# Optimization experiments

Measured on AMD Instinct MI355X. Metric: run time of the kernel, lower is better.

Reference implementation:

```python
import jax, jax.numpy as jnp
from jax import lax
import numpy as np

B, C_IN, C_OUT, H, W = 4, 256, 256, 64, 64
P = 4
DM = C_IN // P            # 64, d_model per parallel chunk
D_STATE = 16
D_CONV = 4
EXPAND = 2
D_INNER = EXPAND * DM     # 128
DT_RANK = max(1, -(-DM // 16))  # ceil(64/16) = 4


def setup_inputs() -> dict:
    key = jax.random.key(0)
    ks = jax.random.split(key, 12)
    s = lambda k, shape, scale=0.02: (jax.random.normal(k, shape, jnp.float32) * scale)
    dt = jax.random.uniform(ks[5], (D_INNER,), jnp.float32, 1e-3, 0.1)
    dt_bias = jnp.log(jnp.expm1(dt))  # inverse softplus, as in mamba_ssm init
    A_log = jnp.log(jnp.tile(jnp.arange(1, D_STATE + 1, dtype=jnp.float32), (D_INNER, 1)))
    return {
        "x": jax.random.normal(ks[0], (B, C_IN, H, W), jnp.float32),
        "ln_g": jnp.ones((C_IN,), jnp.float32),
        "ln_b": jnp.zeros((C_IN,), jnp.float32),
        "in_proj_w": s(ks[1], (2 * D_INNER, DM)),
        "conv_w": s(ks[2], (D_INNER, D_CONV), 0.1),
        "conv_b": jnp.zeros((D_INNER,), jnp.float32),
        "x_proj_w": s(ks[3], (DT_RANK + 2 * D_STATE, D_INNER)),
        "dt_proj_w": s(ks[4], (D_INNER, DT_RANK), 0.1),
        "dt_proj_b": dt_bias,
        "A_log": A_log,
        "D": jnp.ones((D_INNER,), jnp.float32),
        "out_proj_w": s(ks[6], (DM, D_INNER)),
        "skip_scale": jnp.ones((1,), jnp.float32),
        "proj_w": s(ks[7], (C_OUT, C_IN)),
        "proj_b": jnp.zeros((C_OUT,), jnp.float32),
        "cdc_w": s(ks[8], (C_OUT, 1, 3, 3), 0.1),      # depthwise 3x3, groups=C_OUT
        "theta_w": jnp.zeros((1, C_OUT), jnp.float32),  # nn.init.constant_(weight, 0)
        "theta_b": jnp.full((1,), -2.0, jnp.float32),   # nn.init.constant_(bias, -2)
        "pw_w": s(ks[9], (C_OUT, C_OUT)),               # 1x1 pointwise conv, no bias
    }


def _layernorm(x, g, b, eps=1e-5):
    mu = x.mean(-1, keepdims=True)
    var = ((x - mu) ** 2).mean(-1, keepdims=True)
    return (x - mu) * lax.rsqrt(var + eps) * g + b


def _mamba(x, in_proj_w, conv_w, conv_b, x_proj_w, dt_proj_w, dt_proj_b, A_log, D, out_proj_w):
    # x: [Bm, L, DM]
    xz = jnp.einsum('bld,ed->ble', x, in_proj_w)          # [Bm, L, 2*D_INNER]
    xc, z = jnp.split(xz, 2, axis=-1)
    # causal depthwise conv1d along L
    xt = jnp.swapaxes(xc, 1, 2)                           # [Bm, D_INNER, L]
    xt = lax.conv_general_dilated(xt, conv_w[:, None, :], (1,), [(D_CONV - 1, 0)],
                                  dimension_numbers=('NCH', 'OIH', 'NCH'),
                                  feature_group_count=D_INNER)
    xt = xt + conv_b[None, :, None]
    xs = jax.nn.silu(jnp.swapaxes(xt, 1, 2))              # [Bm, L, D_INNER]
    x_dbl = jnp.einsum('bld,ed->ble', xs, x_proj_w)       # [Bm, L, DT_RANK+2*D_STATE]
    dt, Bmat, Cmat = jnp.split(x_dbl, [DT_RANK, DT_RANK + D_STATE], axis=-1)
    delta = jax.nn.softplus(jnp.einsum('blr,dr->bld', dt, dt_proj_w) + dt_proj_b)
    A = -jnp.exp(A_log)                                   # [D_INNER, D_STATE]

    def step(h, inp):
        d_t, b_t, c_t, u_t = inp                          # [Bm,di],[Bm,ds],[Bm,ds],[Bm,di]
        h = h * jnp.exp(d_t[..., None] * A) + (d_t * u_t)[..., None] * b_t[:, None, :]
        return h, jnp.einsum('bds,bs->bd', h, c_t)

    h0 = jnp.zeros((x.shape[0], D_INNER, D_STATE), x.dtype)
    xs_t = (jnp.swapaxes(delta, 0, 1), jnp.swapaxes(Bmat, 0, 1),
            jnp.swapaxes(Cmat, 0, 1), jnp.swapaxes(xs, 0, 1))
    _, ys = lax.scan(step, h0, xs_t)                      # ys: [L, Bm, D_INNER]
    y = jnp.swapaxes(ys, 0, 1) + xs * D
    y = y * jax.nn.silu(z)
    return jnp.einsum('bld,od->blo', y, out_proj_w)       # [Bm, L, DM]


def reference(x, ln_g, ln_b, in_proj_w, conv_w, conv_b, x_proj_w, dt_proj_w, dt_proj_b,
              A_log, D, out_proj_w, skip_scale, proj_w, proj_b, cdc_w, theta_w, theta_b, pw_w):
    Bb, C = x.shape[:2]
    Hh, Ww = x.shape[2], x.shape[3]
    L = Hh * Ww
    x_flat = jnp.swapaxes(x.reshape(Bb, C, L), 1, 2)      # [B, L, C]
    x_norm = _layernorm(x_flat, ln_g, ln_b)
    # chunk along channel dim into P pieces, run shared Mamba on all as one big batch
    xc = jnp.moveaxis(x_norm.reshape(Bb, L, P, DM), 2, 0).reshape(P * Bb, L, DM)
    ym = _mamba(xc, in_proj_w, conv_w, conv_b, x_proj_w, dt_proj_w, dt_proj_b,
                A_log, D, out_proj_w) + skip_scale * xc
    ym = jnp.moveaxis(ym.reshape(P, Bb, L, DM), 0, 2).reshape(Bb, L, C)
    ym = _layernorm(ym, ln_g, ln_b)                       # same norm params (shared)
    yp = jnp.einsum('blc,oc->blo', ym, proj_w) + proj_b
    out = jnp.swapaxes(yp, 1, 2).reshape(Bb, C_OUT, Hh, Ww)
    # A_CDC: depthwise 3x3 conv + central-difference term
    out_normal = lax.conv_general_dilated(out, cdc_w, (1, 1), [(1, 1), (1, 1)],
                                          dimension_numbers=('NCHW', 'OIHW', 'NCHW'),
                                          feature_group_count=C_OUT)
    ksum = cdc_w.sum(axis=(2, 3))[:, 0]                   # [C_OUT]; depthwise 1x1 == scale
    edge = out_normal - out * ksum[None, :, None, None]
    theta = jax.nn.sigmoid(jnp.einsum('bchw,oc->bohw', out, theta_w)
                           + theta_b[None, :, None, None])
    cdc_out = out_normal + theta * edge
    g = jax.nn.gelu(cdc_out, approximate=False)           # nn.GELU exact
    cnn_out = jnp.einsum('bchw,oc->bohw', g, pw_w)        # 1x1 conv, no bias
    return out + cnn_out
```

## Files before the change

kernel.cpp:

```cpp
#include <hip/hip_runtime.h>
#include <hip/hip_bf16.h>
#include <math.h>

typedef __hip_bfloat16 bf16;
typedef short bf8_t __attribute__((ext_vector_type(8)));
typedef float f4_t  __attribute__((ext_vector_type(4)));
typedef float f2_t  __attribute__((ext_vector_type(2)));
#define MFMA16(a,b,c) __builtin_amdgcn_mfma_f32_16x16x32_bf16(a,b,c,0,0,0)
#define DEV __device__ __forceinline__

DEV float bf2f(bf16 h){ return __bfloat162float(h); }
DEV bf16 f2bf(float f){ return __float2bfloat16(f); }
DEV float ld(const void* p, size_t i, int md){
  return md ? ((const float*)p)[i] : bf2f(((const bf16*)p)[i]);
}
DEV float wred(float v){
  #pragma unroll
  for(int off=32; off>0; off>>=1) v += __shfl_down(v, off, 64);
  return __shfl(v, 0, 64);
}

__global__ __launch_bounds__(256) void k_detect(const unsigned short* __restrict__ xr, int* __restrict__ flag){
  __shared__ float sm[4];
  int t = threadIdx.x;
  float m = 0.f;
  for(int i=t;i<8192;i+=256){
    unsigned int w = ((unsigned int)xr[i]) << 16;
    float v = fabsf(__uint_as_float(w));
    if(v != v) v = 1e30f;
    m = fmaxf(m, v);
  }
  #pragma unroll
  for(int off=32; off>0; off>>=1) m = fmaxf(m, __shfl_down(m, off, 64));
  if((t & 63) == 0) sm[t >> 6] = m;
  __syncthreads();
  if(t == 0){
    float mm = fmaxf(fmaxf(sm[0], sm[1]), fmaxf(sm[2], sm[3]));
    *flag = (mm > 1e10f) ? 1 : 0;
  }
}

__global__ __launch_bounds__(256) void k_wcvt(const void* __restrict__ inw, const void* __restrict__ outw,
                                              const void* __restrict__ projw, const void* __restrict__ pww,
                                              bf16* __restrict__ dst, const int* __restrict__ modep){
  const int md = *modep;
  int g = blockIdx.x*256 + threadIdx.x;
  if(g >= 155648) return;
  const void* src; int i;
  if(g < 16384){ src = inw;   i = g; }
  else if(g < 24576){ src = outw;  i = g - 16384; }
  else if(g < 90112){ src = projw; i = g - 24576; }
  else { src = pww; i = g - 90112; }
  dst[g] = f2bf(ld(src, (size_t)i, md));
}

__global__ __launch_bounds__(256) void k_ln1(const void* __restrict__ x, const void* __restrict__ gam,
                                             const void* __restrict__ bet, bf16* __restrict__ xnb,
                                             const int* __restrict__ modep){
  __shared__ float sh[64*257];
  __shared__ float mus[64], rss[64];
  const int md = *modep;
  int t = threadIdx.x;
  int b = blockIdx.x >> 6, lt = blockIdx.x & 63;
  int l0 = lt << 6;
  int lane = t & 63, cg = t >> 6;
  size_t xbase = ((size_t)b << 20) + l0 + lane;
  if(md){
    const float* xp = (const float*)x + xbase;
    #pragma unroll 8
    for(int c = cg; c < 256; c += 4)
      sh[lane*257 + c] = xp[(size_t)c << 12];
  } else {
    const bf16* xp = (const bf16*)x + xbase;
    #pragma unroll 8
    for(int c = cg; c < 256; c += 4)
      sh[lane*257 + c] = bf2f(xp[(size_t)c << 12]);
  }
  __syncthreads();
  {
    int row = t >> 2, q = t & 3;
    const float* rp = sh + row*257 + q*64;
    float s = 0.f, s2 = 0.f;
    #pragma unroll 8
    for(int i=0;i<64;i++){ float v = rp[i]; s += v; s2 += v*v; }
    s  += __shfl_xor(s, 1, 64);  s2 += __shfl_xor(s2, 1, 64);
    s  += __shfl_xor(s, 2, 64);  s2 += __shfl_xor(s2, 2, 64);
    if(q == 0){
      float mu = s*(1.f/256.f);
      mus[row] = mu;
      rss[row] = rsqrtf(s2*(1.f/256.f) - mu*mu + 1e-5f);
    }
  }
  __syncthreads();
  int r0 = (t >> 6) << 4;
  #pragma unroll
  for(int k=0;k<4;k++){
    int c = (t & 63) + (k << 6);
    float gv = ld(gam, c, md), bv = ld(bet, c, md);
    #pragma unroll 4
    for(int rr=0; rr<16; rr++){
      int row = r0 + rr;
      xnb[((size_t)(b*4096 + l0 + row))*256 + c] =
        f2bf((sh[row*257 + c] - mus[row])*rss[row]*gv + bv);
    }
  }
}

__global__ __launch_bounds__(256) void k_inproj(const bf16* __restrict__ xnb, const bf16* __restrict__ wb,
                                                bf16* __restrict__ xcb, bf16* __restrict__ zb){
  __shared__ bf16 As[64*72];
  __shared__ bf16 Ws[256*72];
  int t = threadIdx.x;
  int bm = blockIdx.x >> 6, lt = blockIdx.x & 63;
  int p = bm >> 2, b = bm & 3, l0 = lt << 6;
  #pragma unroll
  for(int pass=0; pass<2; pass++){
    int idx = t + pass*256, r = idx >> 3, ch = idx & 7;
    *(uint4*)&As[r*72 + ch*8] = *(const uint4*)&xnb[((size_t)(b*4096 + l0 + r))*256 + p*64 + ch*8];
  }
  #pragma unroll
  for(int pass=0; pass<8; pass++){
    int idx = t + pass*256, e = idx >> 3, ch = idx & 7;
    *(uint4*)&Ws[e*72 + ch*8] = *(const uint4*)&wb[(size_t)e*64 + ch*8];
  }
  __syncthreads();
  int lane = t & 63, w = t >> 6, quad = lane >> 4, lr = lane & 15;
  f4_t acc[16];
  #pragma unroll
  for(int nt=0;nt<16;nt++) acc[nt] = (f4_t){0.f,0.f,0.f,0.f};
  #pragma unroll
  for(int kk=0; kk<64; kk+=32){
    bf8_t a = *(const bf8_t*)&As[(w*16 + lr)*72 + kk + quad*8];
    #pragma unroll
    for(int nt=0;nt<16;nt++){
      bf8_t bb = *(const bf8_t*)&Ws[(nt*16 + lr)*72 + kk + quad*8];
      acc[nt] = MFMA16(a, bb, acc[nt]);
    }
  }
  __syncthreads();
  bf16* Sl = Ws;
  #pragma unroll
  for(int nt=0;nt<16;nt++)
    #pragma unroll
    for(int r=0;r<4;r++)
      Sl[(w*16 + quad*4 + r)*264 + nt*16 + lr] = f2bf(acc[nt][r]);
  __syncthreads();
  #pragma unroll
  for(int pass=0; pass<8; pass++){
    int idx = t + pass*256, l = idx >> 5, c16 = idx & 31;
    int e0 = c16*8;
    uint4 v = *(uint4*)&Sl[l*264 + e0];
    size_t row = (size_t)bm*4096 + l0 + l;
    if(e0 < 128) *(uint4*)&xcb[row*128 + e0] = v;
    else         *(uint4*)&zb[row*128 + e0 - 128] = v;
  }
}

__global__ __launch_bounds__(256) void k_conv(const bf16* __restrict__ xcb, const void* __restrict__ cw,
                                              const void* __restrict__ cb, bf16* __restrict__ xsb,
                                              const int* __restrict__ modep){
  const int md = *modep;
  int g = blockIdx.x*256 + threadIdx.x;
  int d = g & 127;
  int t4 = g >> 7;
  int l4 = t4 & 1023;
  int bm = t4 >> 10;
  int l0 = l4 << 2;
  size_t base = ((size_t)bm*4096 + l0)*128 + d;
  const bf16* p = xcb + base;
  float w0 = ld(cw,(size_t)(d<<2)+0,md), w1 = ld(cw,(size_t)(d<<2)+1,md);
  float w2 = ld(cw,(size_t)(d<<2)+2,md), w3 = ld(cw,(size_t)(d<<2)+3,md);
  float bv = ld(cb,(size_t)d,md);
  float xm3, xm2, xm1;
  if(l4 > 0){ xm3 = bf2f(p[-384]); xm2 = bf2f(p[-256]); xm1 = bf2f(p[-128]); }
  else      { xm3 = 0.f; xm2 = 0.f; xm1 = 0.f; }
  float x0 = bf2f(p[0]), x1 = bf2f(p[128]), x2 = bf2f(p[256]), x3 = bf2f(p[384]);
  float y0 = fmaf(w0,xm3, fmaf(w1,xm2, fmaf(w2,xm1, fmaf(w3,x0, bv))));
  float y1 = fmaf(w0,xm2, fmaf(w1,xm1, fmaf(w2,x0,  fmaf(w3,x1, bv))));
  float y2 = fmaf(w0,xm1, fmaf(w1,x0,  fmaf(w2,x1,  fmaf(w3,x2, bv))));
  float y3 = fmaf(w0,x0,  fmaf(w1,x1,  fmaf(w2,x2,  fmaf(w3,x3, bv))));
  bf16* o = xsb + base;
  o[0]   = f2bf(y0 / (1.f + __expf(-y0)));
  o[128] = f2bf(y1 / (1.f + __expf(-y1)));
  o[256] = f2bf(y2 / (1.f + __expf(-y2)));
  o[384] = f2bf(y3 / (1.f + __expf(-y3)));
}

#define PTREE2(P, e1) \
  float e2s=(e1)*(e1), e4s=e2s*e2s, e8s=e4s*e4s; \
  f2_t P##0={(e1),e2s}; \
  f2_t P##1=P##0*(f2_t){e2s,e2s}; \
  f2_t e4v_={e4s,e4s}; f2_t P##2=P##0*e4v_, P##3=P##1*e4v_; \
  f2_t e8v_={e8s,e8s}; f2_t P##4=P##0*e8v_, P##5=P##1*e8v_, P##6=P##2*e8v_, P##7=P##3*e8v_;

__global__ __launch_bounds__(256) void k_cxs1(const bf16* __restrict__ xsb, const void* __restrict__ xpw,
                                              float* __restrict__ xdbl,
                                              const void* __restrict__ dtw, const void* __restrict__ dtb,
                                              const void* __restrict__ Alog,
                                              float* __restrict__ CP, bf16* __restrict__ CSb,
                                              const int* __restrict__ modep){
  __shared__ bf16 As[64*136];
  __shared__ bf16 Ws[64*136];
  float* sh = (float*)Ws;
  const int md = *modep;
  int t = threadIdx.x;
  int bm = blockIdx.x >> 6, lt = blockIdx.x & 63;
  size_t row0g = (size_t)bm*4096 + (lt << 6);
  #pragma unroll
  for(int pass=0; pass<4; pass++){
    int idx = t + pass*256, r = idx >> 4, ch = idx & 15;
    *(uint4*)&As[r*136 + ch*8] = *(const uint4*)&xsb[(row0g + r)*128 + ch*8];
  }
  for(int idx = t; idx < 8192; idx += 256){
    int e = idx >> 7, k = idx & 127;
    Ws[e*136 + k] = (e < 36) ? f2bf(ld(xpw, (size_t)e*128 + k, md)) : f2bf(0.f);
  }
  __syncthreads();
  int lane = t & 63, w = t >> 6, quad = lane >> 4, lr = lane & 15;
  f4_t acc[3];
  #pragma unroll
  for(int nt=0;nt<3;nt++) acc[nt] = (f4_t){0.f,0.f,0.f,0.f};
  #pragma unroll
  for(int kk=0; kk<128; kk+=32){
    bf8_t a = *(const bf8_t*)&As[(w*16 + lr)*136 + kk + quad*8];
    #pragma unroll
    for(int nt=0;nt<3;nt++){
      bf8_t bb = *(const bf8_t*)&Ws[(nt*16 + lr)*136 + kk + quad*8];
      acc[nt] = MFMA16(a, bb, acc[nt]);
    }
  }
  __syncthreads();
  #pragma unroll
  for(int nt=0;nt<3;nt++){
    int e = nt*16 + lr;
    if(e < 36){
      #pragma unroll
      for(int r=0;r<4;r++){
        int row = w*16 + quad*4 + r;
        float v = acc[nt][r];
        sh[row*36 + e] = v;
        xdbl[(row0g + row)*36 + e] = v;
      }
    }
  }
  int d = t & 127, chunk = t >> 7;
  float A[16];
  #pragma unroll
  for(int s=0;s<16;s++) A[s] = -expf(ld(Alog, (size_t)((d<<4)+s), md));
  float A0 = A[0];
  int fastf = 1;
  #pragma unroll
  for(int s=0;s<16;s++){
    float n = (float)(s+1);
    if(fabsf(A[s] - n*A0) > 2e-3f*fabsf(n*A0)) fastf = 0;
  }
  fastf = __all(fastf);
  float wdt[4];
  #pragma unroll
  for(int j=0;j<4;j++) wdt[j] = ld(dtw, (size_t)((d<<2)+j), md);
  float bdt = ld(dtb, (size_t)d, md);
  __syncthreads();
  f2_t h2[8];
  #pragma unroll
  for(int j=0;j<8;j++) h2[j] = (f2_t){0.f,0.f};
  float sumd = 0.f;
  const float* shc = sh + chunk*32*36;
  const bf16* uc = As + chunk*32*136;
  if(fastf){
    #pragma unroll
    for(int tt=0;tt<32;tt++){
      const float* r = shc + tt*36;
      float4 dt4 = *(const float4*)r;
      float v = fmaf(dt4.x,wdt[0], fmaf(dt4.y,wdt[1], fmaf(dt4.z,wdt[2], fmaf(dt4.w,wdt[3], bdt))));
      float dv = fmaxf(v,0.f) + __logf(1.f + __expf(-fabsf(v)));
      float u = bf2f(uc[tt*136 + d]);
      float du = dv*u; sumd += dv;
      const f2_t* B2 = (const f2_t*)(r+4);
      float e1 = __expf(dv*A0);
      PTREE2(p, e1);
      f2_t du2 = {du,du};
      h2[0] = h2[0]*p0 + du2*B2[0];
      h2[1] = h2[1]*p1 + du2*B2[1];
      h2[2] = h2[2]*p2 + du2*B2[2];
      h2[3] = h2[3]*p3 + du2*B2[3];
      h2[4] = h2[4]*p4 + du2*B2[4];
      h2[5] = h2[5]*p5 + du2*B2[5];
      h2[6] = h2[6]*p6 + du2*B2[6];
      h2[7] = h2[7]*p7 + du2*B2[7];
    }
  } else {
    for(int tt=0;tt<32;tt++){
      const float* r = shc + tt*36;
      float4 dt4 = *(const float4*)r;
      float v = fmaf(dt4.x,wdt[0], fmaf(dt4.y,wdt[1], fmaf(dt4.z,wdt[2], fmaf(dt4.w,wdt[3], bdt))));
      float dv = fmaxf(v,0.f) + __logf(1.f + __expf(-fabsf(v)));
      float u = bf2f(uc[tt*136 + d]);
      float du = dv*u; sumd += dv;
      const float* Bp = r + 4;
      #pragma unroll
      for(int j=0;j<8;j++){
        f2_t e = { __expf(dv*A[2*j]), __expf(dv*A[2*j+1]) };
        f2_t bb = { Bp[2*j], Bp[2*j+1] };
        h2[j] = h2[j]*e + (f2_t){du,du}*bb;
      }
    }
  }
  int c = lt*2 + chunk;
  size_t ob = ((size_t)(bm*128 + c)*128 + d) << 4;
  if(fastf){
    float qv = __expf(sumd*A0);
    PTREE2(P, qv);
    *(f2_t*)&CP[ob+ 0]=P0; *(f2_t*)&CP[ob+ 2]=P1; *(f2_t*)&CP[ob+ 4]=P2; *(f2_t*)&CP[ob+ 6]=P3;
    *(f2_t*)&CP[ob+ 8]=P4; *(f2_t*)&CP[ob+10]=P5; *(f2_t*)&CP[ob+12]=P6; *(f2_t*)&CP[ob+14]=P7;
  } else {
    #pragma unroll
    for(int s=0;s<16;s++) CP[ob+s] = __expf(sumd*A[s]);
  }
  __align__(16) bf16 pk[8];
  #pragma unroll
  for(int j=0;j<4;j++){ pk[2*j] = f2bf(h2[j].x); pk[2*j+1] = f2bf(h2[j].y); }
  *(uint4*)&CSb[ob] = *(uint4*)pk;
  #pragma unroll
  for(int j=0;j<4;j++){ pk[2*j] = f2bf(h2[4+j].x); pk[2*j+1] = f2bf(h2[4+j].y); }
  *(uint4*)&CSb[ob+8] = *(uint4*)pk;
}

__global__ __launch_bounds__(64) void k_scan2(float* __restrict__ CP, const bf16* __restrict__ CSb){
  int g = blockIdx.x*64 + threadIdx.x;
  int bm = g >> 11, ds = g & 2047;
  size_t base = ((size_t)bm << 18) + ds;
  float Pb[8], Sb[8];
  #pragma unroll
  for(int j=0;j<8;j++){
    size_t idx = base + ((size_t)j << 11);
    Pb[j] = CP[idx]; Sb[j] = bf2f(CSb[idx]);
  }
  float h = 0.f;
  #pragma unroll
  for(int grp=0; grp<16; grp++){
    float Pc[8], Sc[8];
    #pragma unroll
    for(int j=0;j<8;j++){ Pc[j]=Pb[j]; Sc[j]=Sb[j]; }
    if(grp < 15){
      #pragma unroll
      for(int j=0;j<8;j++){
        size_t idx = base + ((size_t)((grp+1)*8 + j) << 11);
        Pb[j] = CP[idx]; Sb[j] = bf2f(CSb[idx]);
      }
    }
    #pragma unroll
    for(int j=0;j<8;j++){
      size_t idx = base + ((size_t)(grp*8 + j) << 11);
      CP[idx] = h;
      h = fmaf(Pc[j], h, Sc[j]);
    }
  }
}

__global__ __launch_bounds__(128) void k_scan3(bf16* __restrict__ zb, const bf16* __restrict__ xsb,
                                               const float* __restrict__ xdbl,
                                               const void* __restrict__ dtw, const void* __restrict__ dtb,
                                               const void* __restrict__ Alog, const void* __restrict__ Dw,
                                               const float* __restrict__ CP, const int* __restrict__ modep){
  __shared__ float sh[32*36];
  __shared__ bf16 su[32*128];
  const int md = *modep;
  int d = threadIdx.x;
  int bm = blockIdx.x >> 7, c = blockIdx.x & 127;
  size_t row0 = (size_t)bm*4096 + (c<<5);
  {
    const float4* src = (const float4*)(xdbl + row0*36);
    for(int idx = d; idx < 288; idx += 128) ((float4*)sh)[idx] = src[idx];
    const uint4* gu = (const uint4*)(xsb + row0*128);
    uint4* lu = (uint4*)su;
    #pragma unroll
    for(int j=0;j<4;j++) lu[d + j*128] = gu[d + j*128];
  }
  float A[16];
  #pragma unroll
  for(int s=0;s<16;s++) A[s] = -expf(ld(Alog, (size_t)((d<<4)+s), md));
  float A0 = A[0];
  int fastf = 1;
  #pragma unroll
  for(int s=0;s<16;s++){
    float n = (float)(s+1);
    if(fabsf(A[s] - n*A0) > 2e-3f*fabsf(n*A0)) fastf = 0;
  }
  fastf = __all(fastf);
  float wdt[4];
  #pragma unroll
  for(int j=0;j<4;j++) wdt[j] = ld(dtw, (size_t)((d<<2)+j), md);
  float bdt = ld(dtb, (size_t)d, md);
  float Dd = ld(Dw, (size_t)d, md);
  size_t hb = ((size_t)(bm*128 + c)*128 + d) << 4;
  f2_t h2[8];
  #pragma unroll
  for(int j=0;j<8;j++) h2[j] = *(const f2_t*)&CP[hb + 2*j];
  __syncthreads();
  if(fastf){
    #pragma unroll
    for(int tt=0;tt<32;tt++){
      const float* r = sh + tt*36;
      size_t bg = (row0 + tt)*128 + d;
      float zv = bf2f(zb[bg]);
      float4 dt4 = *(const float4*)r;
      float v = fmaf(dt4.x,wdt[0], fmaf(dt4.y,wdt[1], fmaf(dt4.z,wdt[2], fmaf(dt4.w,wdt[3], bdt))));
      float dv = fmaxf(v,0.f) + __logf(1.f + __expf(-fabsf(v)));
      float u  = bf2f(su[tt*128 + d]);
      float du = dv*u;
      const f2_t* B2 = (const f2_t*)(r+4);
      const f2_t* C2 = (const f2_t*)(r+20);
      float e1 = __expf(dv*A0);
      PTREE2(p, e1);
      f2_t du2 = {du,du};
      f2_t ya = {0.f,0.f}, yb = {0.f,0.f};
      h2[0] = h2[0]*p0 + du2*B2[0];  ya += h2[0]*C2[0];
      h2[1] = h2[1]*p1 + du2*B2[1];  yb += h2[1]*C2[1];
      h2[2] = h2[2]*p2 + du2*B2[2];  ya += h2[2]*C2[2];
      h2[3] = h2[3]*p3 + du2*B2[3];  yb += h2[3]*C2[3];
      h2[4] = h2[4]*p4 + du2*B2[4];  ya += h2[4]*C2[4];
      h2[5] = h2[5]*p5 + du2*B2[5];  yb += h2[5]*C2[5];
      h2[6] = h2[6]*p6 + du2*B2[6];  ya += h2[6]*C2[6];
      h2[7] = h2[7]*p7 + du2*B2[7];  yb += h2[7]*C2[7];
      float y = (ya.x + ya.y) + (yb.x + yb.y);
      float yv = (y + u*Dd) * (zv / (1.f + __expf(-zv)));
      zb[bg] = f2bf(yv);
    }
  } else {
    for(int tt=0;tt<32;tt++){
      const float* r = sh + tt*36;
      size_t bg = (row0 + tt)*128 + d;
      float zv = bf2f(zb[bg]);
      float4 dt4 = *(const float4*)r;
      float v = fmaf(dt4.x,wdt[0], fmaf(dt4.y,wdt[1], fmaf(dt4.z,wdt[2], fmaf(dt4.w,wdt[3], bdt))));
      float dv = fmaxf(v,0.f) + __logf(1.f + __expf(-fabsf(v)));
      float u  = bf2f(su[tt*128 + d]);
      float du = dv*u;
      const float* Bp = r + 4;
      const float* Cp = r + 20;
      f2_t ya = {0.f,0.f};
      #pragma unroll
      for(int j=0;j<8;j++){
        f2_t e = { __expf(dv*A[2*j]), __expf(dv*A[2*j+1]) };
        f2_t bb = { Bp[2*j], Bp[2*j+1] };
        f2_t cc = { Cp[2*j], Cp[2*j+1] };
        h2[j] = h2[j]*e + (f2_t){du,du}*bb;
        ya += h2[j]*cc;
      }
      float y = ya.x + ya.y;
      float yv = (y + u*Dd) * (zv / (1.f + __expf(-zv)));
      zb[bg] = f2bf(yv);
    }
  }
}

__global__ __launch_bounds__(256) void k_outproj(const bf16* __restrict__ yb, const bf16* __restrict__ xnb,
                                                 const bf16* __restrict__ wb, const void* __restrict__ ss,
                                                 bf16* __restrict__ ymb, const int* __restrict__ modep){
  __shared__ bf16 As[64*72];
  __shared__ bf16 Ws[64*72];
  const int md = *modep;
  int t = threadIdx.x;
  int bm = blockIdx.x >> 6, lt = blockIdx.x & 63;
  int p = bm >> 2, b = bm & 3, l0 = lt << 6;
  int lane = t & 63, w = t >> 6, quad = lane >> 4, lr = lane & 15;
  f4_t acc[4];
  #pragma unroll
  for(int nt=0;nt<4;nt++) acc[nt] = (f4_t){0.f,0.f,0.f,0.f};
  for(int kb=0; kb<2; kb++){
    if(kb) __syncthreads();
    int k0 = kb << 6;
    #pragma unroll
    for(int pass=0; pass<2; pass++){
      int idx = t + pass*256, r = idx >> 3, ch = idx & 7;
      *(uint4*)&As[r*72 + ch*8] = *(const uint4*)&yb[((size_t)bm*4096 + l0 + r)*128 + k0 + ch*8];
    }
    #pragma unroll
    for(int pass=0; pass<2; pass++){
      int idx = t + pass*256, o = idx >> 3, ch = idx & 7;
      *(uint4*)&Ws[o*72 + ch*8] = *(const uint4*)&wb[(size_t)o*128 + k0 + ch*8];
    }
    __syncthreads();
    #pragma unroll
    for(int kk=0; kk<64; kk+=32){
      bf8_t a = *(const bf8_t*)&As[(w*16 + lr)*72 + kk + quad*8];
      #pragma unroll
      for(int nt=0;nt<4;nt++){
        bf8_t bb = *(const bf8_t*)&Ws[(nt*16 + lr)*72 + kk + quad*8];
        acc[nt] = MFMA16(a, bb, acc[nt]);
      }
    }
  }
  __syncthreads();
  bf16* Sl = As;
  #pragma unroll
  for(int nt=0;nt<4;nt++)
    #pragma unroll
    for(int r=0;r<4;r++)
      Sl[(w*16 + quad*4 + r)*72 + nt*16 + lr] = f2bf(acc[nt][r]);
  __syncthreads();
  float sv = ld(ss, 0, md);
  #pragma unroll
  for(int pass=0; pass<2; pass++){
    int idx = t + pass*256, l = idx >> 3, ch = idx & 7;
    size_t gi = ((size_t)b*4096 + l0 + l)*256 + p*64 + ch*8;
    uint4 yv = *(uint4*)&Sl[l*72 + ch*8];
    uint4 xv = *(const uint4*)&xnb[gi];
    const bf16* y8 = (const bf16*)&yv;
    const bf16* x8 = (const bf16*)&xv;
    uint4 ov; bf16* o8 = (bf16*)&ov;
    #pragma unroll
    for(int j=0;j<8;j++) o8[j] = f2bf(fmaf(sv, bf2f(x8[j]), bf2f(y8[j])));
    *(uint4*)&ymb[gi] = ov;
  }
}

__global__ __launch_bounds__(256) void k_ln2(bf16* __restrict__ ymb, const void* __restrict__ gam,
                                             const void* __restrict__ bet, const int* __restrict__ modep){
  const int md = *modep;
  int lane = threadIdx.x & 63, wv = threadIdx.x >> 6;
  size_t row = (size_t)blockIdx.x*4 + wv;
  bf16* rp = ymb + row*256 + (lane<<2);
  __align__(8) bf16 raw[4];
  *(ushort4*)raw = *(const ushort4*)rp;
  float v[4];
  #pragma unroll
  for(int i=0;i<4;i++) v[i] = bf2f(raw[i]);
  float s = v[0]+v[1]+v[2]+v[3];
  float s2 = v[0]*v[0]+v[1]*v[1]+v[2]*v[2]+v[3]*v[3];
  s = wred(s); s2 = wred(s2);
  float mu = s*(1.f/256.f);
  float rs = rsqrtf(s2*(1.f/256.f) - mu*mu + 1e-5f);
  int c = lane << 2;
  #pragma unroll
  for(int i=0;i<4;i++) raw[i] = f2bf((v[i]-mu)*rs*ld(gam,c+i,md) + ld(bet,c+i,md));
  *(ushort4*)rp = *(ushort4*)raw;
}

__global__ __launch_bounds__(256) void k_proj(const bf16* __restrict__ ymb, const bf16* __restrict__ wb,
                                              const void* __restrict__ pb, bf16* __restrict__ outbb,
                                              const void* __restrict__ tw, const void* __restrict__ tb2,
                                              float* __restrict__ theta, const int* __restrict__ modep){
  __shared__ bf16 As[32*72];
  __shared__ bf16 Ws[256*72];
  const int md = *modep;
  int t = threadIdx.x;
  int row0 = blockIdx.x << 5;
  int b = row0 >> 12, l0 = row0 & 4095;
  int lane = t & 63, w = t >> 6, quad = lane >> 4, lr = lane & 15;
  int rg = w & 1, ch2 = w >> 1;
  f4_t acc[8];
  #pragma unroll
  for(int nt=0;nt<8;nt++) acc[nt] = (f4_t){0.f,0.f,0.f,0.f};
  for(int kb=0; kb<4; kb++){
    if(kb) __syncthreads();
    int k0 = kb << 6;
    { int r = t >> 3, ch = t & 7;
      *(uint4*)&As[r*72 + ch*8] = *(const uint4*)&ymb[((size_t)(row0 + r))*256 + k0 + ch*8]; }
    #pragma unroll
    for(int pass=0; pass<8; pass++){
      int idx = t + pass*256, e = idx >> 3, ch = idx & 7;
      *(uint4*)&Ws[e*72 + ch*8] = *(const uint4*)&wb[(size_t)e*256 + k0 + ch*8];
    }
    __syncthreads();
    #pragma unroll
    for(int kk=0; kk<64; kk+=32){
      bf8_t a = *(const bf8_t*)&As[(rg*16 + lr)*72 + kk + quad*8];
      #pragma unroll
      for(int nt=0;nt<8;nt++){
        bf8_t bb = *(const bf8_t*)&Ws[(ch2*128 + nt*16 + lr)*72 + kk + quad*8];
        acc[nt] = MFMA16(a, bb, acc[nt]);
      }
    }
  }
  __syncthreads();
  bf16* Sl = Ws;
  #pragma unroll
  for(int nt=0;nt<8;nt++){
    int o = ch2*128 + nt*16 + lr;
    float bv = ld(pb, (size_t)o, md);
    #pragma unroll
    for(int r=0;r<4;r++)
      Sl[o*40 + rg*16 + quad*4 + r] = f2bf(acc[nt][r] + bv);
  }
  __syncthreads();
  #pragma unroll
  for(int pass=0; pass<4; pass++){
    int idx = t + pass*256, o = idx >> 2, q = idx & 3;
    uint4 v = *(uint4*)&Sl[o*40 + q*8];
    *(uint4*)&outbb[((size_t)(b*256 + o) << 12) + l0 + q*8] = v;
  }
  if(t < 32){
    float acc2 = 0.f;
    #pragma unroll 8
    for(int o=0;o<256;o++)
      acc2 = fmaf(bf2f(Sl[o*40 + t]), ld(tw, (size_t)o, md), acc2);
    float v = acc2 + ld(tb2, 0, md);
    theta[((size_t)b << 12) + l0 + t] = 1.f / (1.f + __expf(-v));
  }
}

__global__ __launch_bounds__(256) void k_cdc(const bf16* __restrict__ outbb, const float* __restrict__ theta,
                                             const void* __restrict__ cw, bf16* __restrict__ gbufb,
                                             const int* __restrict__ modep){
  const int md = *modep;
  int g = blockIdx.x*256 + threadIdx.x;
  int w4 = g & 15;
  int h0 = (g >> 4) & 63;
  int c  = (g >> 10) & 255;
  int b  = g >> 18;
  int w0 = w4 << 2;
  float wk[9]; float ks = 0.f;
  #pragma unroll
  for(int j=0;j<9;j++){ wk[j] = ld(cw, (size_t)c*9 + j, md); ks += wk[j]; }
  const bf16* base = outbb + (((size_t)b*256 + c) << 12);
  float X[3][6];
  #pragma unroll
  for(int dy=0;dy<3;dy++){
    int hh = h0 + dy - 1;
    #pragma unroll
    for(int dx=0;dx<6;dx++){
      int ww = w0 + dx - 1;
      X[dy][dx] = (hh>=0 && hh<64 && ww>=0 && ww<64) ? bf2f(base[(hh<<6)+ww]) : 0.f;
    }
  }
  float4 th = *(const float4*)&theta[((size_t)b<<12) + (h0<<6) + w0];
  float thv[4] = {th.x, th.y, th.z, th.w};
  __align__(8) bf16 outp[4];
  #pragma unroll
  for(int k=0;k<4;k++){
    float on = 0.f;
    #pragma unroll
    for(int dy=0;dy<3;dy++)
      #pragma unroll
      for(int dx=0;dx<3;dx++)
        on = fmaf(X[dy][k+dx], wk[dy*3+dx], on);
    float ctr  = X[1][k+1];
    float edge = on - ctr*ks;
    float cd   = fmaf(thv[k], edge, on);
    outp[k] = f2bf(0.5f * cd * (1.f + erff(cd * 0.70710678118654752f)));
  }
  *(ushort4*)&gbufb[(((size_t)b*256 + c) << 12) + (h0<<6) + w0] = *(ushort4*)outp;
}

__global__ __launch_bounds__(256) void k_pw(const bf16* __restrict__ gbufb, const bf16* __restrict__ outbb,
                                            const bf16* __restrict__ wb, void* __restrict__ outp,
                                            const int* __restrict__ modep){
  __shared__ bf16 As[64*72];
  __shared__ bf16 Bs[128*72];
  const int md = *modep;
  int t = threadIdx.x;
  int b  = blockIdx.x >> 7;
  int ot = (blockIdx.x >> 5) & 3;
  int ht = blockIdx.x & 31;
  int o0 = ot << 6, hw0 = ht << 7;
  int lane = t & 63, w = t >> 6, quad = lane >> 4, lr = lane & 15;
  f4_t acc[8];
  #pragma unroll
  for(int nt=0;nt<8;nt++) acc[nt] = (f4_t){0.f,0.f,0.f,0.f};
  for(int kb=0; kb<4; kb++){
    if(kb) __syncthreads();
    int k0 = kb << 6;
    #pragma unroll
    for(int pass=0; pass<2; pass++){
      int idx = t + pass*256, r = idx >> 3, ch = idx & 7;
      *(uint4*)&As[r*72 + ch*8] = *(const uint4*)&wb[(size_t)(o0 + r)*256 + k0 + ch*8];
    }
    #pragma unroll
    for(int pass=0; pass<4; pass++){
      int idx = t + pass*256, cc = idx >> 4, hc = idx & 15;
      uint4 gv = *(const uint4*)&gbufb[((size_t)(b*256 + k0 + cc) << 12) + hw0 + hc*8];
      const bf16* g8 = (const bf16*)&gv;
      #pragma unroll
      for(int j=0;j<8;j++) Bs[(hc*8 + j)*72 + cc] = g8[j];
    }
    __syncthreads();
    #pragma unroll
    for(int kk=0; kk<64; kk+=32){
      bf8_t a = *(const bf8_t*)&As[(w*16 + lr)*72 + kk + quad*8];
      #pragma unroll
      for(int nt=0;nt<8;nt++){
        bf8_t bb = *(const bf8_t*)&Bs[(nt*16 + lr)*72 + kk + quad*8];
        acc[nt] = MFMA16(a, bb, acc[nt]);
      }
    }
  }
  __syncthreads();
  bf16* Sl = Bs;
  #pragma unroll
  for(int nt=0;nt<8;nt++)
    #pragma unroll
    for(int r=0;r<4;r++)
      Sl[(w*16 + quad*4 + r)*136 + nt*16 + lr] = f2bf(acc[nt][r]);
  __syncthreads();
  #pragma unroll
  for(int pass=0; pass<4; pass++){
    int idx = t + pass*256, ol = idx >> 4, c16 = idx & 15;
    size_t ro = ((size_t)(b*256 + o0 + ol) << 12) + hw0 + c16*8;
    uint4 sv = *(uint4*)&Sl[ol*136 + c16*8];
    uint4 rv = *(const uint4*)&outbb[ro];
    const bf16* s8 = (const bf16*)&sv;
    const bf16* r8 = (const bf16*)&rv;
    if(md){
      float4 f0, f1;
      f0.x = bf2f(s8[0]) + bf2f(r8[0]); f0.y = bf2f(s8[1]) + bf2f(r8[1]);
      f0.z = bf2f(s8[2]) + bf2f(r8[2]); f0.w = bf2f(s8[3]) + bf2f(r8[3]);
      f1.x = bf2f(s8[4]) + bf2f(r8[4]); f1.y = bf2f(s8[5]) + bf2f(r8[5]);
      f1.z = bf2f(s8[6]) + bf2f(r8[6]); f1.w = bf2f(s8[7]) + bf2f(r8[7]);
      *(float4*)&((float*)outp)[ro]     = f0;
      *(float4*)&((float*)outp)[ro + 4] = f1;
    } else {
      uint4 ov; bf16* o8 = (bf16*)&ov;
      #pragma unroll
      for(int j=0;j<8;j++) o8[j] = f2bf(bf2f(s8[j]) + bf2f(r8[j]));
      *(uint4*)&((bf16*)outp)[ro] = ov;
    }
  }
}

extern "C" void kernel_launch(void* const* d_in, const int* in_sizes, int n_in,
                              void* d_out, int out_size, void* d_ws, size_t ws_size,
                              hipStream_t stream){
  const void* x      = d_in[0];
  const void* ln_g   = d_in[1];
  const void* ln_b   = d_in[2];
  const void* inw    = d_in[3];
  const void* convw  = d_in[4];
  const void* convb  = d_in[5];
  const void* xpw    = d_in[6];
  const void* dtw    = d_in[7];
  const void* dtb    = d_in[8];
  const void* Alog   = d_in[9];
  const void* Dw     = d_in[10];
  const void* outw   = d_in[11];
  const void* sscale = d_in[12];
  const void* projw  = d_in[13];
  const void* projb  = d_in[14];
  const void* cdcw   = d_in[15];
  const void* thw    = d_in[16];
  const void* thb    = d_in[17];
  const void* pww    = d_in[18];
  float* ws = (float*)d_ws;

  bf16*  xnb   = (bf16*)(ws);
  bf16*  xcb   = (bf16*)(ws + 2097152);
  float* CP    = ws + 2097152;
  bf16*  ymb   = (bf16*)(ws + 2097152);
  bf16*  outbb = (bf16*)(ws + 4194304);
  bf16*  zb    = (bf16*)(ws + 6291456);
  bf16*  gbufb = (bf16*)(ws + 6291456);
  bf16*  xsb   = (bf16*)(ws + 10485760);
  float* theta = ws + 10485760;
  float* xdbl  = ws + 14680064;
  int*   flag  = (int*)(ws + 17039360);
  bf16*  wsb   = (bf16*)(ws + 17039364);
  bf16*  inwb  = wsb;
  bf16*  outwb = wsb + 16384;
  bf16*  projwb= wsb + 24576;
  bf16*  pwwb  = wsb + 90112;
  bf16*  CSb   = (bf16*)d_out;

  k_detect <<<1,    256, 0, stream>>>((const unsigned short*)x, flag);
  k_wcvt   <<<608,  256, 0, stream>>>(inw, outw, projw, pww, wsb, flag);
  k_ln1    <<<256,  256, 0, stream>>>(x, ln_g, ln_b, xnb, flag);
  k_inproj <<<1024, 256, 0, stream>>>(xnb, inwb, xcb, zb);
  k_conv   <<<8192, 256, 0, stream>>>(xcb, convw, convb, xsb, flag);
  k_cxs1   <<<1024, 256, 0, stream>>>(xsb, xpw, xdbl, dtw, dtb, Alog, CP, CSb, flag);
  k_scan2  <<<512,  64,  0, stream>>>(CP, CSb);
  k_scan3  <<<2048, 128, 0, stream>>>(zb, xsb, xdbl, dtw, dtb, Alog, Dw, CP, flag);
  k_outproj<<<1024, 256, 0, stream>>>(zb, xnb, outwb, sscale, ymb, flag);
  k_ln2    <<<4096, 256, 0, stream>>>(ymb, ln_g, ln_b, flag);
  k_proj   <<<512,  256, 0, stream>>>(ymb, projwb, projb, outbb, thw, thb, theta, flag);
  k_cdc    <<<4096, 256, 0, stream>>>(outbb, theta, cdcw, gbufb, flag);
  k_pw     <<<512,  256, 0, stream>>>(gbufb, outbb, pwwb, d_out, flag);
}
```

Baseline: 310.3 us.

## Fuse selective scan output with out_proj GEMM and skip-add in one kernel

The scan kernel now keeps its gated output tile (32 timesteps x 128 channels) in shared memory instead of writing it back to the z buffer. It then runs the out_proj MFMA and the skip-scale residual add directly, and the separate out_proj kernel is removed. The shared-memory rows are padded to avoid bank conflicts. This removes a global write and re-read of the scan output and one launch. In exchange, each block reloads the full 64x128 out_proj weight into LDS and uses more shared memory, and ymb now lives in the output buffer.

```diff
diff --git a/kernel.cpp b/kernel.cpp
--- a/kernel.cpp
+++ b/kernel.cpp
@@ -357,16 +357,22 @@
   }
 }
 
-__global__ __launch_bounds__(128) void k_scan3(bf16* __restrict__ zb, const bf16* __restrict__ xsb,
-                                               const float* __restrict__ xdbl,
-                                               const void* __restrict__ dtw, const void* __restrict__ dtb,
-                                               const void* __restrict__ Alog, const void* __restrict__ Dw,
-                                               const float* __restrict__ CP, const int* __restrict__ modep){
+__global__ __launch_bounds__(128) void k_scan3o(const bf16* __restrict__ zb, const bf16* __restrict__ xsb,
+                                                const float* __restrict__ xdbl,
+                                                const void* __restrict__ dtw, const void* __restrict__ dtb,
+                                                const void* __restrict__ Alog, const void* __restrict__ Dw,
+                                                const float* __restrict__ CP,
+                                                const bf16* __restrict__ xnb, const bf16* __restrict__ wout,
+                                                const void* __restrict__ ss, bf16* __restrict__ ymb,
+                                                const int* __restrict__ modep){
   __shared__ float sh[32*36];
-  __shared__ bf16 su[32*128];
-  const int md = *modep;
-  int d = threadIdx.x;
+  __shared__ bf16 su[32*136];
+  __shared__ bf16 Ws[64*136];
+  const int md = *modep;
+  int t = threadIdx.x;
+  int d = t;
   int bm = blockIdx.x >> 7, c = blockIdx.x & 127;
+  int p = bm >> 2, b = bm & 3;
   size_t row0 = (size_t)bm*4096 + (c<<5);
   {
     const float4* src = (const float4*)(xdbl + row0*36);
@@ -374,7 +380,17 @@
     const uint4* gu = (const uint4*)(xsb + row0*128);
     uint4* lu = (uint4*)su;
     #pragma unroll
-    for(int j=0;j<4;j++) lu[d + j*128] = gu[d + j*128];
+    for(int j=0;j<4;j++){
+      int i = d + j*128;
+      lu[(i>>4)*17 + (i&15)] = gu[i];
+    }
+    const uint4* gw = (const uint4*)wout;
+    uint4* lw = (uint4*)Ws;
+    #pragma unroll
+    for(int j=0;j<8;j++){
+      int i = d + j*128;
+      lw[(i>>4)*17 + (i&15)] = gw[i];
+    }
   }
   float A[16];
   #pragma unroll
@@ -406,25 +422,25 @@
       float4 dt4 = *(const float4*)r;
       float v = fmaf(dt4.x,wdt[0], fmaf(dt4.y,wdt[1], fmaf(dt4.z,wdt[2], fmaf(dt4.w,wdt[3], bdt))));
       float dv = fmaxf(v,0.f) + __logf(1.f + __expf(-fabsf(v)));
-      float u  = bf2f(su[tt*128 + d]);
+      float u  = bf2f(su[tt*136 + d]);
       float du = dv*u;
       const f2_t* B2 = (const f2_t*)(r+4);
       const f2_t* C2 = (const f2_t*)(r+20);
       float e1 = __expf(dv*A0);
-      PTREE2(p, e1);
+      PTREE2(p_, e1);
       f2_t du2 = {du,du};
       f2_t ya = {0.f,0.f}, yb = {0.f,0.f};
-      h2[0] = h2[0]*p0 + du2*B2[0];  ya += h2[0]*C2[0];
-      h2[1] = h2[1]*p1 + du2*B2[1];  yb += h2[1]*C2[1];
-      h2[2] = h2[2]*p2 + du2*B2[2];  ya += h2[2]*C2[2];
-      h2[3] = h2[3]*p3 + du2*B2[3];  yb += h2[3]*C2[3];
-      h2[4] = h2[4]*p4 + du2*B2[4];  ya += h2[4]*C2[4];
-      h2[5] = h2[5]*p5 + du2*B2[5];  yb += h2[5]*C2[5];
-      h2[6] = h2[6]*p6 + du2*B2[6];  ya += h2[6]*C2[6];
-      h2[7] = h2[7]*p7 + du2*B2[7];  yb += h2[7]*C2[7];
+      h2[0] = h2[0]*p_0 + du2*B2[0];  ya += h2[0]*C2[0];
+      h2[1] = h2[1]*p_1 + du2*B2[1];  yb += h2[1]*C2[1];
+      h2[2] = h2[2]*p_2 + du2*B2[2];  ya += h2[2]*C2[2];
+      h2[3] = h2[3]*p_3 + du2*B2[3];  yb += h2[3]*C2[3];
+      h2[4] = h2[4]*p_4 + du2*B2[4];  ya += h2[4]*C2[4];
+      h2[5] = h2[5]*p_5 + du2*B2[5];  yb += h2[5]*C2[5];
+      h2[6] = h2[6]*p_6 + du2*B2[6];  ya += h2[6]*C2[6];
+      h2[7] = h2[7]*p_7 + du2*B2[7];  yb += h2[7]*C2[7];
       float y = (ya.x + ya.y) + (yb.x + yb.y);
       float yv = (y + u*Dd) * (zv / (1.f + __expf(-zv)));
-      zb[bg] = f2bf(yv);
+      su[tt*136 + d] = f2bf(yv);
     }
   } else {
     for(int tt=0;tt<32;tt++){
@@ -434,7 +450,7 @@
       float4 dt4 = *(const float4*)r;
       float v = fmaf(dt4.x,wdt[0], fmaf(dt4.y,wdt[1], fmaf(dt4.z,wdt[2], fmaf(dt4.w,wdt[3], bdt))));
       float dv = fmaxf(v,0.f) + __logf(1.f + __expf(-fabsf(v)));
-      float u  = bf2f(su[tt*128 + d]);
+      float u  = bf2f(su[tt*136 + d]);
       float du = dv*u;
       const float* Bp = r + 4;
       const float* Cp = r + 20;
@@ -449,50 +465,24 @@
       }
       float y = ya.x + ya.y;
       float yv = (y + u*Dd) * (zv / (1.f + __expf(-zv)));
-      zb[bg] = f2bf(yv);
-    }
-  }
-}
-
-__global__ __launch_bounds__(256) void k_outproj(const bf16* __restrict__ yb, const bf16* __restrict__ xnb,
-                                                 const bf16* __restrict__ wb, const void* __restrict__ ss,
-                                                 bf16* __restrict__ ymb, const int* __restrict__ modep){
-  __shared__ bf16 As[64*72];
-  __shared__ bf16 Ws[64*72];
-  const int md = *modep;
-  int t = threadIdx.x;
-  int bm = blockIdx.x >> 6, lt = blockIdx.x & 63;
-  int p = bm >> 2, b = bm & 3, l0 = lt << 6;
+      su[tt*136 + d] = f2bf(yv);
+    }
+  }
+  __syncthreads();
   int lane = t & 63, w = t >> 6, quad = lane >> 4, lr = lane & 15;
   f4_t acc[4];
   #pragma unroll
   for(int nt=0;nt<4;nt++) acc[nt] = (f4_t){0.f,0.f,0.f,0.f};
-  for(int kb=0; kb<2; kb++){
-    if(kb) __syncthreads();
-    int k0 = kb << 6;
-    #pragma unroll
-    for(int pass=0; pass<2; pass++){
-      int idx = t + pass*256, r = idx >> 3, ch = idx & 7;
-      *(uint4*)&As[r*72 + ch*8] = *(const uint4*)&yb[((size_t)bm*4096 + l0 + r)*128 + k0 + ch*8];
-    }
-    #pragma unroll
-    for(int pass=0; pass<2; pass++){
-      int idx = t + pass*256, o = idx >> 3, ch = idx & 7;
-      *(uint4*)&Ws[o*72 + ch*8] = *(const uint4*)&wb[(size_t)o*128 + k0 + ch*8];
-    }
-    __syncthreads();
-    #pragma unroll
-    for(int kk=0; kk<64; kk+=32){
-      bf8_t a = *(const bf8_t*)&As[(w*16 + lr)*72 + kk + quad*8];
-      #pragma unroll
-      for(int nt=0;nt<4;nt++){
-        bf8_t bb = *(const bf8_t*)&Ws[(nt*16 + lr)*72 + kk + quad*8];
-        acc[nt] = MFMA16(a, bb, acc[nt]);
-      }
-    }
-  }
-  __syncthreads();
-  bf16* Sl = As;
+  #pragma unroll
+  for(int kk=0; kk<128; kk+=32){
+    bf8_t a = *(const bf8_t*)&su[(w*16 + lr)*136 + kk + quad*8];
+    #pragma unroll
+    for(int nt=0;nt<4;nt++){
+      bf8_t bb = *(const bf8_t*)&Ws[(nt*16 + lr)*136 + kk + quad*8];
+      acc[nt] = MFMA16(a, bb, acc[nt]);
+    }
+  }
+  bf16* Sl = (bf16*)sh;
   #pragma unroll
   for(int nt=0;nt<4;nt++)
     #pragma unroll
@@ -502,9 +492,10 @@
   float sv = ld(ss, 0, md);
   #pragma unroll
   for(int pass=0; pass<2; pass++){
-    int idx = t + pass*256, l = idx >> 3, ch = idx & 7;
-    size_t gi = ((size_t)b*4096 + l0 + l)*256 + p*64 + ch*8;
-    uint4 yv = *(uint4*)&Sl[l*72 + ch*8];
+    int idx = t + pass*128;
+    int row = idx >> 3, ch = idx & 7;
+    size_t gi = ((size_t)b*4096 + (c<<5) + row)*256 + p*64 + ch*8;
+    uint4 yv = *(uint4*)&Sl[row*72 + ch*8];
     uint4 xv = *(const uint4*)&xnb[gi];
     const bf16* y8 = (const bf16*)&yv;
     const bf16* x8 = (const bf16*)&xv;
@@ -745,7 +736,6 @@
   bf16*  xnb   = (bf16*)(ws);
   bf16*  xcb   = (bf16*)(ws + 2097152);
   float* CP    = ws + 2097152;
-  bf16*  ymb   = (bf16*)(ws + 2097152);
   bf16*  outbb = (bf16*)(ws + 4194304);
   bf16*  zb    = (bf16*)(ws + 6291456);
   bf16*  gbufb = (bf16*)(ws + 6291456);
@@ -759,6 +749,7 @@
   bf16*  projwb= wsb + 24576;
   bf16*  pwwb  = wsb + 90112;
   bf16*  CSb   = (bf16*)d_out;
+  bf16*  ymb   = (bf16*)d_out;
 
   k_detect <<<1,    256, 0, stream>>>((const unsigned short*)x, flag);
   k_wcvt   <<<608,  256, 0, stream>>>(inw, outw, projw, pww, wsb, flag);
@@ -767,8 +758,8 @@
   k_conv   <<<8192, 256, 0, stream>>>(xcb, convw, convb, xsb, flag);
   k_cxs1   <<<1024, 256, 0, stream>>>(xsb, xpw, xdbl, dtw, dtb, Alog, CP, CSb, flag);
   k_scan2  <<<512,  64,  0, stream>>>(CP, CSb);
-  k_scan3  <<<2048, 128, 0, stream>>>(zb, xsb, xdbl, dtw, dtb, Alog, Dw, CP, flag);
-  k_outproj<<<1024, 256, 0, stream>>>(zb, xnb, outwb, sscale, ymb, flag);
+  k_scan3o <<<2048, 128, 0, stream>>>(zb, xsb, xdbl, dtw, dtb, Alog, Dw, CP,
+                                      xnb, outwb, sscale, ymb, flag);
   k_ln2    <<<4096, 256, 0, stream>>>(ymb, ln_g, ln_b, flag);
   k_proj   <<<512,  256, 0, stream>>>(ymb, projwb, projb, outbb, thw, thb, theta, flag);
   k_cdc    <<<4096, 256, 0, stream>>>(outbb, theta, cdcw, gbufb, flag);
```

After: 306.7 us. About the same (-1.2%).
